# Optimization experiments

Hardware: AMD Instinct MI355X
Metric: run time of the kernel (lower is better)

## Reference

```python
import jax, jax.numpy as jnp
import numpy as np

N = 100000   # nodes
E = 3200000  # edges (avg degree 32)
IN, H, OUT = 128, 256, 40
EPS = 1e-5


def _glorot(key, fan_in, fan_out):
    s = jnp.sqrt(2.0 / (fan_in + fan_out))
    return jax.random.normal(key, (fan_in, fan_out), jnp.float32) * s


def setup_inputs() -> dict:
    key = jax.random.key(0)
    ks = jax.random.split(key, 6)
    edge_index = jax.random.randint(ks[0], (2, E), 0, N, dtype=jnp.int64)
    z = jax.random.normal(ks[1], (N, IN), jnp.float32) * 0.1
    return {
        "edge_index": edge_index,
        "z": z,
        "W1": _glorot(ks[2], IN, H), "b1": jnp.zeros((H,), jnp.float32),
        "g1": jnp.ones((H,), jnp.float32), "beta1": jnp.zeros((H,), jnp.float32),
        "W2": _glorot(ks[3], H, H), "b2": jnp.zeros((H,), jnp.float32),
        "g2": jnp.ones((H,), jnp.float32), "beta2": jnp.zeros((H,), jnp.float32),
        "W3": _glorot(ks[4], H, OUT), "b3": jnp.zeros((OUT,), jnp.float32),
    }


def _gcn_norm(edge_index):
    # add self-loops, compute symmetric normalization D^-1/2 (A+I) D^-1/2
    loops = jnp.arange(N, dtype=edge_index.dtype)
    src = jnp.concatenate([edge_index[0], loops])
    dst = jnp.concatenate([edge_index[1], loops])
    deg = jax.ops.segment_sum(jnp.ones_like(dst, jnp.float32), dst, num_segments=N)
    dinv = jnp.where(deg > 0, jax.lax.rsqrt(deg), 0.0)
    norm = dinv[src] * dinv[dst]  # [E+N]
    return src, dst, norm


def _conv(x, W, b, src, dst, norm):
    h = x @ W                              # [N, F_out]
    msg = h[src] * norm[:, None]           # gather + scale, [E+N, F_out]
    return jax.ops.segment_sum(msg, dst, num_segments=N) + b


def _bn(x, g, beta):
    m = x.mean(axis=0)
    v = x.var(axis=0)  # biased variance (training-mode BatchNorm)
    return (x - m) * jax.lax.rsqrt(v + EPS) * g + beta


def reference(edge_index, z, W1, b1, g1, beta1, W2, b2, g2, beta2, W3, b3):
    src, dst, norm = _gcn_norm(edge_index)
    x = jax.nn.relu(_bn(_conv(z, W1, b1, src, dst, norm), g1, beta1))
    x = jax.nn.relu(_bn(_conv(x, W2, b2, src, dst, norm), g2, beta2))
    return _conv(x, W3, b3, src, dst, norm)  # [N, OUT]
```

## Files before the change

### kernel.cpp

```cpp
#include <hip/hip_runtime.h>


#define NN   100000
#define NE   3200000
#define FIN  128
#define FH   256
#define FOUT 40
#define EPSV 1e-5f

#define BSH   7
#define NBKT  ((NN + 127) >> BSH)
#define CAPB  8192
#define CHNK  4096

typedef __attribute__((ext_vector_type(8))) short bf8;
typedef __attribute__((ext_vector_type(4))) float f32x4;

__device__ __forceinline__ unsigned short f2bf(float x) {
    unsigned int u = __float_as_uint(x);
    unsigned int r = u + 0x7fffu + ((u >> 16) & 1u);
    return (unsigned short)(r >> 16);
}
__device__ __forceinline__ float bf2f(unsigned short h) {
    return __uint_as_float(((unsigned int)h) << 16);
}
__device__ __forceinline__ void f2bf2(float x, unsigned short& hi, unsigned short& lo) {
    unsigned short h = f2bf(x);
    hi = h;
    lo = f2bf(x - bf2f(h));
}
__device__ __forceinline__ float ub(unsigned int u, int k) {
    return (float)((u >> (8 * k)) & 0xffu);
}
__device__ __forceinline__ float sbyte(unsigned int u, int k) {
    return (float)(int)(signed char)((u >> (8 * k)) & 0xffu);
}

__global__ __launch_bounds__(256) void k_bin(const int* __restrict__ ei,
                                             int* __restrict__ gcur,
                                             unsigned int* __restrict__ staging) {
    __shared__ int hcnt[NBKT];
    __shared__ int hbase[NBKT];
    __shared__ int sflag;
    const int tid = threadIdx.x;
    const int e0 = blockIdx.x * CHNK;
    for (int b = tid; b < NBKT; b += 256) hcnt[b] = 0;
    if (tid == 0) {
        int zz = 0;
        for (int i = 0; i < 64; i++) zz |= ei[2 * i + 1];
        sflag = (zz == 0) ? 1 : 0;
    }
    __syncthreads();
    const int f = sflag;
    for (int r = 0; r < CHNK / 256; r++) {
        int e = e0 + r * 256 + tid;
        if (e < NE) {
            int d = f ? ei[2 * (NE + e)] : ei[NE + e];
            atomicAdd(&hcnt[d >> BSH], 1);
        }
    }
    __syncthreads();
    for (int b = tid; b < NBKT; b += 256) {
        int c = hcnt[b];
        hbase[b] = c ? atomicAdd(&gcur[b], c) : 0;
    }
    __syncthreads();
    for (int b = tid; b < NBKT; b += 256) hcnt[b] = 0;
    __syncthreads();
    for (int r = 0; r < CHNK / 256; r++) {
        int e = e0 + r * 256 + tid;
        if (e < NE) {
            int s = f ? ei[2 * e] : ei[e];
            int d = f ? ei[2 * (NE + e)] : ei[NE + e];
            int b = d >> BSH;
            int loc = atomicAdd(&hcnt[b], 1);
            int pos = hbase[b] + loc;
            if (pos < CAPB)
                staging[(size_t)b * CAPB + pos] =
                    (unsigned int)s | ((unsigned int)(d & 127) << 17);
        }
    }
}

__global__ void k_bucketscan(const int* __restrict__ gcur, int* __restrict__ bbase) {
    __shared__ int sb2[2][256];
    int t = threadIdx.x;
    int base = t * 4;
    int v0 = (base + 0 < NBKT) ? gcur[base + 0] : 0;
    int v1 = (base + 1 < NBKT) ? gcur[base + 1] : 0;
    int v2 = (base + 2 < NBKT) ? gcur[base + 2] : 0;
    int v3 = (base + 3 < NBKT) ? gcur[base + 3] : 0;
    int s0 = v0, s1 = s0 + v1, s2 = s1 + v2, s3 = s2 + v3;
    sb2[0][t] = s3;
    __syncthreads();
    int pi = 0;
    for (int off = 1; off < 256; off <<= 1) {
        int x = sb2[pi][t];
        if (t >= off) x += sb2[pi][t - off];
        sb2[pi ^ 1][t] = x;
        __syncthreads();
        pi ^= 1;
    }
    int excl = sb2[pi][t] - s3;
    if (base + 0 < NBKT) bbase[base + 0] = excl;
    if (base + 1 < NBKT) bbase[base + 1] = excl + s0;
    if (base + 2 < NBKT) bbase[base + 2] = excl + s1;
    if (base + 3 < NBKT) bbase[base + 3] = excl + s2;
}

__global__ __launch_bounds__(256) void k_build(const unsigned int* __restrict__ staging,
                                               const int* __restrict__ gcur,
                                               const int* __restrict__ bbase,
                                               int* __restrict__ cntg,
                                               float* __restrict__ dinv,
                                               int* __restrict__ rowptr,
                                               int* __restrict__ csr) {
    __shared__ int lcnt[128];
    __shared__ int lscan[2][128];
    __shared__ int lcur[128];
    const int tid = threadIdx.x;
    const int b = blockIdx.x;
    const int tot = min(gcur[b], CAPB);
    const int bb = bbase[b];
    const unsigned int* st = staging + (size_t)b * CAPB;
    if (tid < 128) lcnt[tid] = 0;
    __syncthreads();
    for (int i = tid; i < tot; i += 256) {
        unsigned int v = st[i];
        atomicAdd(&lcnt[v >> 17], 1);
    }
    __syncthreads();
    int pi = 0;
    if (tid < 128) lscan[0][tid] = lcnt[tid];
    __syncthreads();
    for (int off = 1; off < 128; off <<= 1) {
        if (tid < 128) {
            int x = lscan[pi][tid];
            if (tid >= off) x += lscan[pi][tid - off];
            lscan[pi ^ 1][tid] = x;
        }
        __syncthreads();
        pi ^= 1;
    }
    if (tid < 128) {
        int c = lcnt[tid];
        int excl = lscan[pi][tid] - c;
        lcur[tid] = excl;
        int node = (b << BSH) + tid;
        if (node < NN) {
            cntg[node] = c;
            dinv[node] = rsqrtf((float)(c + 1));
            rowptr[node] = bb + excl;
        }
    }
    __syncthreads();
    for (int i = tid; i < tot; i += 256) {
        unsigned int v = st[i];
        int pos = atomicAdd(&lcur[v >> 17], 1);
        csr[bb + pos] = (int)(v & 0x1ffffu);
    }
}

__global__ void k_wprep(const float* __restrict__ W1, unsigned short* __restrict__ W1h,
                        unsigned short* __restrict__ W1l,
                        const float* __restrict__ W2, unsigned short* __restrict__ W2h,
                        unsigned short* __restrict__ W2l,
                        const float* __restrict__ W3, unsigned short* __restrict__ W3h,
                        unsigned short* __restrict__ W3l) {
    int idx = blockIdx.x * blockDim.x + threadIdx.x;
    const float* W;
    unsigned short *Wh, *Wl;
    int K, M, MP;
    if (idx < 256 * 128) {
        W = W1; Wh = W1h; Wl = W1l; K = 128; M = 256; MP = 256;
    } else if (idx < 256 * 128 + 256 * 256) {
        idx -= 256 * 128;
        W = W2; Wh = W2h; Wl = W2l; K = 256; M = 256; MP = 256;
    } else if (idx < 256 * 128 + 256 * 256 + 64 * 256) {
        idx -= 256 * 128 + 256 * 256;
        W = W3; Wh = W3h; Wl = W3l; K = 256; M = 40; MP = 64;
    } else {
        return;
    }
    int m = idx / K, k = idx - m * K;
    float v = (m < M) ? W[(size_t)k * M + m] : 0.f;
    unsigned short h, l;
    f2bf2(v, h, l);
    size_t dst = ((size_t)(k >> 5) * MP + m) * 32 + (k & 31);
    Wh[dst] = h;
    Wl[dst] = l;
}

__global__ __launch_bounds__(256) void k_zpb8(const float* __restrict__ z,
                                              const float* __restrict__ dinv,
                                              unsigned char* __restrict__ zp8,
                                              float* __restrict__ scaleZ) {
    int wv = (blockIdx.x * blockDim.x + threadIdx.x) >> 6;
    int lane = threadIdx.x & 63;
    if (wv >= NN) return;
    float2 v = *(const float2*)(z + (size_t)wv * FIN + lane * 2);
    float d = dinv[wv];
    float a0 = v.x * d, a1 = v.y * d;
    float m = fmaxf(fabsf(a0), fabsf(a1));
#pragma unroll
    for (int off = 1; off < 64; off <<= 1) m = fmaxf(m, __shfl_xor(m, off));
    float inv = m > 0.f ? 127.f / m : 0.f;
    int q0 = (int)rintf(a0 * inv), q1 = (int)rintf(a1 * inv);
    unsigned short pk = (unsigned short)((q0 & 0xff) | ((q1 & 0xff) << 8));
    *(unsigned short*)(zp8 + (size_t)wv * FIN + lane * 2) = pk;
    if (lane == 0) scaleZ[wv] = m * (1.f / 127.f);
}

__global__ __launch_bounds__(256) void k_bnr8(const unsigned short* __restrict__ x,
                                              const float* __restrict__ scale,
                                              const float* __restrict__ shift,
                                              const float* __restrict__ dinv,
                                              unsigned char* __restrict__ y8,
                                              float* __restrict__ scaleY) {
    int wv = (blockIdx.x * blockDim.x + threadIdx.x) >> 6;
    int lane = threadIdx.x & 63;
    if (wv >= NN) return;
    uint2 u = *(const uint2*)(x + (size_t)wv * 256 + lane * 4);
    float4 sc = *(const float4*)(scale + lane * 4);
    float4 sh = *(const float4*)(shift + lane * 4);
    float d = dinv[wv];
    float v0 = fmaxf(__uint_as_float(u.x << 16) * sc.x + sh.x, 0.f) * d;
    float v1 = fmaxf(__uint_as_float(u.x & 0xffff0000u) * sc.y + sh.y, 0.f) * d;
    float v2 = fmaxf(__uint_as_float(u.y << 16) * sc.z + sh.z, 0.f) * d;
    float v3 = fmaxf(__uint_as_float(u.y & 0xffff0000u) * sc.w + sh.w, 0.f) * d;
    float m = fmaxf(fmaxf(v0, v1), fmaxf(v2, v3));
#pragma unroll
    for (int off = 1; off < 64; off <<= 1) m = fmaxf(m, __shfl_xor(m, off));
    float inv = m > 0.f ? 255.f / m : 0.f;
    unsigned int q0 = (unsigned int)(v0 * inv + 0.5f);
    unsigned int q1 = (unsigned int)(v1 * inv + 0.5f);
    unsigned int q2 = (unsigned int)(v2 * inv + 0.5f);
    unsigned int q3 = (unsigned int)(v3 * inv + 0.5f);
    *(unsigned int*)(y8 + (size_t)wv * 256 + lane * 4) = q0 | (q1 << 8) | (q2 << 16) | (q3 << 24);
    if (lane == 0) scaleY[wv] = m * (1.f / 255.f);
}

template <int F, bool SIGNED>
__global__ __launch_bounds__(256) void k_agg8(const unsigned char* __restrict__ tab,
                                              const float* __restrict__ rscale,
                                              const float* __restrict__ dinv,
                                              const int* __restrict__ rowptr,
                                              const int* __restrict__ cnt,
                                              const int* __restrict__ csr,
                                              unsigned short* __restrict__ oa) {
    const int wid = threadIdx.x >> 6;
    const int lane = threadIdx.x & 63;
    const int wstep = (blockDim.x >> 6) * gridDim.x;
    constexpr int B = F / 64;
    const int off = lane * B;
    for (int row0 = blockIdx.x * (blockDim.x >> 6) + wid; row0 < NN; row0 += wstep) {
        const int row = __builtin_amdgcn_readfirstlane(row0);
        const int rp = __builtin_amdgcn_readfirstlane(rowptr[row]);
        const int cn = __builtin_amdgcn_readfirstlane(cnt[row]);
        float acc[B];
        {
            float s = rscale[row];
            if constexpr (B == 4) {
                unsigned int u = *(const unsigned int*)(tab + (size_t)row * F + off);
                acc[0] = s * ub(u, 0); acc[1] = s * ub(u, 1);
                acc[2] = s * ub(u, 2); acc[3] = s * ub(u, 3);
            } else {
                unsigned int u = *(const unsigned short*)(tab + (size_t)row * F + off);
                acc[0] = s * sbyte(u, 0); acc[1] = s * sbyte(u, 1);
            }
        }
        int e = 0;
        for (; e + 8 <= cn; e += 8) {
            int idx[8];
            float s[8];
            unsigned int u[8];
#pragma unroll
            for (int j = 0; j < 8; j++) idx[j] = csr[rp + e + j];
#pragma unroll
            for (int j = 0; j < 8; j++) s[j] = rscale[idx[j]];
#pragma unroll
            for (int j = 0; j < 8; j++) {
                if constexpr (B == 4)
                    u[j] = *(const unsigned int*)(tab + (size_t)idx[j] * F + off);
                else
                    u[j] = *(const unsigned short*)(tab + (size_t)idx[j] * F + off);
            }
#pragma unroll
            for (int j = 0; j < 8; j++) {
                if constexpr (B == 4) {
                    acc[0] += s[j] * ub(u[j], 0); acc[1] += s[j] * ub(u[j], 1);
                    acc[2] += s[j] * ub(u[j], 2); acc[3] += s[j] * ub(u[j], 3);
                } else {
                    acc[0] += s[j] * sbyte(u[j], 0); acc[1] += s[j] * sbyte(u[j], 1);
                }
            }
        }
        for (; e < cn; e++) {
            int idx = csr[rp + e];
            float s = rscale[idx];
            if constexpr (B == 4) {
                unsigned int u = *(const unsigned int*)(tab + (size_t)idx * F + off);
                acc[0] += s * ub(u, 0); acc[1] += s * ub(u, 1);
                acc[2] += s * ub(u, 2); acc[3] += s * ub(u, 3);
            } else {
                unsigned int u = *(const unsigned short*)(tab + (size_t)idx * F + off);
                acc[0] += s * sbyte(u, 0); acc[1] += s * sbyte(u, 1);
            }
        }
        float d = dinv[row];
        size_t p = (size_t)row * F + off;
        if constexpr (B == 4) {
            uint2 o;
            o.x = (unsigned int)f2bf(acc[0] * d) | ((unsigned int)f2bf(acc[1] * d) << 16);
            o.y = (unsigned int)f2bf(acc[2] * d) | ((unsigned int)f2bf(acc[3] * d) << 16);
            *(uint2*)(oa + p) = o;
        } else {
            *(unsigned int*)(oa + p) =
                (unsigned int)f2bf(acc[0] * d) | ((unsigned int)f2bf(acc[1] * d) << 16);
        }
    }
}

template <int K>
__global__ __launch_bounds__(256) void k_gemm(const unsigned short* __restrict__ A,
                                              const unsigned short* __restrict__ Wth,
                                              const unsigned short* __restrict__ Wtl,
                                              const float* __restrict__ bias,
                                              unsigned short* __restrict__ outX,
                                              float* __restrict__ s1,
                                              float* __restrict__ s2) {
    __shared__ unsigned short sA[64][40];
    const int t = threadIdx.x;
    const int w = t >> 6, lane = t & 63;
    const int quad = lane >> 4, l16 = lane & 15;
    const int rowBase = blockIdx.y * 64;
    const int colW = blockIdx.x * 128 + w * 32;
    f32x4 acc[4][2];
#pragma unroll
    for (int i = 0; i < 4; i++)
#pragma unroll
        for (int j = 0; j < 2; j++) acc[i][j] = (f32x4)0.f;

    for (int k0 = 0; k0 < K; k0 += 32) {
        int gr = rowBase + (t >> 2);
        int4 v = {0, 0, 0, 0};
        if (gr < NN) v = *(const int4*)(A + (size_t)gr * K + k0 + (t & 3) * 8);
        __syncthreads();
        *(int4*)&sA[t >> 2][(t & 3) * 8] = v;
        __syncthreads();
        const int kb = k0 >> 5;
        bf8 bh[2], bl[2];
#pragma unroll
        for (int j = 0; j < 2; j++) {
            size_t bo = ((size_t)(kb * 256 + colW + j * 16 + l16)) * 32 + quad * 8;
            bh[j] = *(const bf8*)(Wth + bo);
            bl[j] = *(const bf8*)(Wtl + bo);
        }
#pragma unroll
        for (int i = 0; i < 4; i++) {
            bf8 a = *(const bf8*)&sA[i * 16 + l16][quad * 8];
#pragma unroll
            for (int j = 0; j < 2; j++) {
                acc[i][j] = __builtin_amdgcn_mfma_f32_16x16x32_bf16(a, bh[j], acc[i][j], 0, 0, 0);
                acc[i][j] = __builtin_amdgcn_mfma_f32_16x16x32_bf16(a, bl[j], acc[i][j], 0, 0, 0);
            }
        }
    }
#pragma unroll
    for (int j = 0; j < 2; j++) {
        int col = colW + j * 16 + l16;
        float b = bias[col];
        float s1p = 0.f, s2p = 0.f;
#pragma unroll
        for (int i = 0; i < 4; i++) {
#pragma unroll
            for (int r = 0; r < 4; r++) {
                int row = rowBase + i * 16 + quad * 4 + r;
                if (row < NN) {
                    float v = acc[i][j][r] + b;
                    s1p += v;
                    s2p += v * v;
                    outX[(size_t)row * 256 + col] = f2bf(v);
                }
            }
        }
        s1p += __shfl_xor(s1p, 16); s1p += __shfl_xor(s1p, 32);
        s2p += __shfl_xor(s2p, 16); s2p += __shfl_xor(s2p, 32);
        if (quad == 0) {
            atomicAdd(&s1[col], s1p);
            atomicAdd(&s2[col], s2p);
        }
    }
}

__global__ __launch_bounds__(256) void k_mgemm3(const unsigned short* __restrict__ y2,
                                                const unsigned short* __restrict__ Wth,
                                                const unsigned short* __restrict__ Wtl,
                                                unsigned char* __restrict__ H8,
                                                float* __restrict__ scaleH) {
    __shared__ unsigned short sA[128][40];
    __shared__ float sM[128][4];
    const int t = threadIdx.x;
    const int w = t >> 6, lane = t & 63;
    const int quad = lane >> 4, l16 = lane & 15;
    const int rowBase = blockIdx.x << 7;
    f32x4 acc[8];
#pragma unroll
    for (int i = 0; i < 8; i++) acc[i] = (f32x4)0.f;

    for (int k0 = 0; k0 < 256; k0 += 32) {
        const int kb = k0 >> 5;
        int id0 = t, id1 = t + 256;
        int gr0 = rowBase + (id0 >> 2), gr1 = rowBase + (id1 >> 2);
        int4 zz = {0, 0, 0, 0};
        int4 v0 = (gr0 < NN) ? *(const int4*)(y2 + (size_t)gr0 * 256 + k0 + (id0 & 3) * 8) : zz;
        int4 v1 = (gr1 < NN) ? *(const int4*)(y2 + (size_t)gr1 * 256 + k0 + (id1 & 3) * 8) : zz;
        __syncthreads();
        *(int4*)&sA[id0 >> 2][(id0 & 3) * 8] = v0;
        *(int4*)&sA[id1 >> 2][(id1 & 3) * 8] = v1;
        __syncthreads();
        size_t bo = ((size_t)(kb * 64 + w * 16 + l16)) * 32 + quad * 8;
        bf8 bh = *(const bf8*)(Wth + bo);
        bf8 bl = *(const bf8*)(Wtl + bo);
#pragma unroll
        for (int i = 0; i < 8; i++) {
            bf8 a = *(const bf8*)&sA[i * 16 + l16][quad * 8];
            acc[i] = __builtin_amdgcn_mfma_f32_16x16x32_bf16(a, bh, acc[i], 0, 0, 0);
            acc[i] = __builtin_amdgcn_mfma_f32_16x16x32_bf16(a, bl, acc[i], 0, 0, 0);
        }
    }
#pragma unroll
    for (int i = 0; i < 8; i++) {
#pragma unroll
        for (int r = 0; r < 4; r++) {
            float m = fabsf(acc[i][r]);
            m = fmaxf(m, __shfl_xor(m, 1));
            m = fmaxf(m, __shfl_xor(m, 2));
            m = fmaxf(m, __shfl_xor(m, 4));
            m = fmaxf(m, __shfl_xor(m, 8));
            if (l16 == 0) sM[i * 16 + quad * 4 + r][w] = m;
        }
    }
    __syncthreads();
    const int col = w * 16 + l16;
#pragma unroll
    for (int i = 0; i < 8; i++) {
#pragma unroll
        for (int r = 0; r < 4; r++) {
            int rloc = i * 16 + quad * 4 + r;
            int row = rowBase + rloc;
            float m = fmaxf(fmaxf(sM[rloc][0], sM[rloc][1]), fmaxf(sM[rloc][2], sM[rloc][3]));
            float inv = m > 0.f ? 127.f / m : 0.f;
            if (row < NN) {
                int q = (int)rintf(acc[i][r] * inv);
                H8[(size_t)row * 64 + col] = (unsigned char)(q & 0xff);
                if (w == 0 && l16 == 0) scaleH[row] = m * (1.f / 127.f);
            }
        }
    }
}

__global__ __launch_bounds__(256) void k_aggfb8(const unsigned char* __restrict__ tab,
                                                const float* __restrict__ rscale,
                                                const float* __restrict__ dinv,
                                                const int* __restrict__ rowptr,
                                                const int* __restrict__ cnt,
                                                const int* __restrict__ csr,
                                                const float* __restrict__ bias,
                                                float* __restrict__ out) {
    const int wid = threadIdx.x >> 6;
    const int lane = threadIdx.x & 63;
    const int wstep = (blockDim.x >> 6) * gridDim.x;
    for (int row0 = blockIdx.x * (blockDim.x >> 6) + wid; row0 < NN; row0 += wstep) {
        const int row = __builtin_amdgcn_readfirstlane(row0);
        const int rp = __builtin_amdgcn_readfirstlane(rowptr[row]);
        const int cn = __builtin_amdgcn_readfirstlane(cnt[row]);
        float acc = rscale[row] * (float)(int)(signed char)tab[(size_t)row * 64 + lane];
        int e = 0;
        for (; e + 8 <= cn; e += 8) {
            int idx[8];
            float s[8];
            float v[8];
#pragma unroll
            for (int j = 0; j < 8; j++) idx[j] = csr[rp + e + j];
#pragma unroll
            for (int j = 0; j < 8; j++) s[j] = rscale[idx[j]];
#pragma unroll
            for (int j = 0; j < 8; j++)
                v[j] = (float)(int)(signed char)tab[(size_t)idx[j] * 64 + lane];
#pragma unroll
            for (int j = 0; j < 8; j++) acc += s[j] * v[j];
        }
        for (; e < cn; e++) {
            int idx = csr[rp + e];
            float s = rscale[idx];
            acc += s * (float)(int)(signed char)tab[(size_t)idx * 64 + lane];
        }
        if (lane < FOUT) out[(size_t)row * FOUT + lane] = acc * dinv[row] + bias[lane];
    }
}

__global__ void k_bnfold(const float* __restrict__ s1, const float* __restrict__ s2,
                         const float* __restrict__ g, const float* __restrict__ be,
                         float* __restrict__ scale, float* __restrict__ shift) {
    int c = threadIdx.x;
    if (c < 256) {
        float mean = s1[c] * (1.f / NN);
        float var = s2[c] * (1.f / NN) - mean * mean;
        float sc = g[c] * rsqrtf(var + EPSV);
        scale[c] = sc;
        shift[c] = be[c] - mean * sc;
    }
}

__global__ void k_bnr(const unsigned short* __restrict__ x,
                      const float* __restrict__ scale, const float* __restrict__ shift,
                      const float* __restrict__ dinv, unsigned short* __restrict__ oy) {
    int i = blockIdx.x * blockDim.x + threadIdx.x;
    if (i >= NN * 128) return;
    int row = i >> 7;
    int c = (i & 127) * 2;
    unsigned int u = ((const unsigned int*)x)[i];
    float x0 = __uint_as_float(u << 16);
    float x1 = __uint_as_float(u & 0xffff0000u);
    float d = dinv[row];
    float v0 = fmaxf(x0 * scale[c + 0] + shift[c + 0], 0.f) * d;
    float v1 = fmaxf(x1 * scale[c + 1] + shift[c + 1], 0.f) * d;
    ((unsigned int*)oy)[i] = (unsigned int)f2bf(v0) | ((unsigned int)f2bf(v1) << 16);
}

extern "C" void kernel_launch(void* const* d_in, const int* in_sizes, int n_in,
                              void* d_out, int out_size, void* d_ws, size_t ws_size,
                              hipStream_t stream) {
    const int* ei = (const int*)d_in[0];
    const float* z = (const float*)d_in[1];
    const float* W1 = (const float*)d_in[2];
    const float* b1 = (const float*)d_in[3];
    const float* g1 = (const float*)d_in[4];
    const float* be1 = (const float*)d_in[5];
    const float* W2 = (const float*)d_in[6];
    const float* b2 = (const float*)d_in[7];
    const float* g2 = (const float*)d_in[8];
    const float* be2 = (const float*)d_in[9];
    const float* W3 = (const float*)d_in[10];
    const float* b3 = (const float*)d_in[11];
    float* out = (float*)d_out;

    char* w = (char*)d_ws;
    size_t o = 0;
    auto take = [&](size_t bytes) {
        char* p = w + o;
        o = (o + bytes + 255) & ~(size_t)255;
        return p;
    };
    int* cnt = (int*)take((size_t)NN * 4);
    int* rowptr = (int*)take((size_t)NN * 4);
    int* gcur = (int*)take(NBKT * 4);
    int* bbase = (int*)take(NBKT * 4);
    int* csr = (int*)take((size_t)NE * 4);
    unsigned int* staging = (unsigned int*)take((size_t)NBKT * CAPB * 4);
    float* dinv = (float*)take((size_t)NN * 4);
    float* stat = (float*)take(4 * 256 * 4);
    float* sc1 = (float*)take(256 * 4);
    float* sh1 = (float*)take(256 * 4);
    float* sc2 = (float*)take(256 * 4);
    float* sh2 = (float*)take(256 * 4);
    unsigned short* Wt1h = (unsigned short*)take(256 * 128 * 2);
    unsigned short* Wt1l = (unsigned short*)take(256 * 128 * 2);
    unsigned short* Wt2h = (unsigned short*)take(256 * 256 * 2);
    unsigned short* Wt2l = (unsigned short*)take(256 * 256 * 2);
    unsigned short* Wt3h = (unsigned short*)take(64 * 256 * 2);
    unsigned short* Wt3l = (unsigned short*)take(64 * 256 * 2);
    unsigned char* zp8 = (unsigned char*)take((size_t)NN * FIN);
    unsigned char* y1_8 = (unsigned char*)take((size_t)NN * FH);
    unsigned char* H8 = (unsigned char*)take((size_t)NN * 64);
    float* scaleZ = (float*)take((size_t)NN * 4);
    float* scaleY = (float*)take((size_t)NN * 4);
    float* scaleH = (float*)take((size_t)NN * 4);
    unsigned short* P1 = (unsigned short*)take((size_t)NN * 256 * 2);
    unsigned short* P2 = (unsigned short*)take((size_t)NN * 512 * 2);

    unsigned short* a1 = P1;
    unsigned short* x1 = P2;
    unsigned short* a2 = P2 + (size_t)NN * 256;
    unsigned short* x2 = P1;
    unsigned short* y2 = P2;
    float* s1a = stat, *s2a = stat + 256, *s1b = stat + 512, *s2b = stat + 768;

    hipMemsetAsync(gcur, 0, NBKT * 4, stream);
    hipMemsetAsync(stat, 0, 4 * 256 * 4, stream);

    k_bin<<<(NE + CHNK - 1) / CHNK, 256, 0, stream>>>(ei, gcur, staging);
    k_bucketscan<<<1, 256, 0, stream>>>(gcur, bbase);
    k_build<<<NBKT, 256, 0, stream>>>(staging, gcur, bbase, cnt, dinv, rowptr, csr);

    k_wprep<<<(256 * 128 + 256 * 256 + 64 * 256 + 255) / 256, 256, 0, stream>>>(
        W1, Wt1h, Wt1l, W2, Wt2h, Wt2l, W3, Wt3h, Wt3l);

    const int GR = (NN + 63) / 64;
    const int WV = (NN + 3) / 4;

    k_zpb8<<<WV, 256, 0, stream>>>(z, dinv, zp8, scaleZ);
    k_agg8<128, true><<<2560, 256, 0, stream>>>(zp8, scaleZ, dinv, rowptr, cnt, csr, a1);
    k_gemm<128><<<dim3(2, GR), 256, 0, stream>>>(a1, Wt1h, Wt1l, b1, x1, s1a, s2a);
    k_bnfold<<<1, 256, 0, stream>>>(s1a, s2a, g1, be1, sc1, sh1);
    k_bnr8<<<WV, 256, 0, stream>>>(x1, sc1, sh1, dinv, y1_8, scaleY);

    k_agg8<256, false><<<2560, 256, 0, stream>>>(y1_8, scaleY, dinv, rowptr, cnt, csr, a2);
    k_gemm<256><<<dim3(2, GR), 256, 0, stream>>>(a2, Wt2h, Wt2l, b2, x2, s1b, s2b);
    k_bnfold<<<1, 256, 0, stream>>>(s1b, s2b, g2, be2, sc2, sh2);
    k_bnr<<<(NN * 128 + 255) / 256, 256, 0, stream>>>(x2, sc2, sh2, dinv, y2);

    k_mgemm3<<<NBKT, 256, 0, stream>>>(y2, Wt3h, Wt3l, H8, scaleH);
    k_aggfb8<<<2560, 256, 0, stream>>>(H8, scaleH, dinv, rowptr, cnt, csr, b3, out);
}
```

Before: 815.8 us.

## Fuse BN folding into consumers and pipeline two-row edge aggregation

Removes the k_bnfold launches by computing BN scale/shift inline in k_bnr8 and k_mgemm3. The second BN+ReLU pass (k_bnr) is fused into the final GEMM's A-tile load, which drops a full intermediate write and read. The aggregation kernels now process two rows per wave with double-buffered 8-edge batches so gathers overlap with FMAs. The padded batches waste some loads on self-rows, and register pressure goes up.

```diff
diff --git a/kernel.cpp b/kernel.cpp
--- a/kernel.cpp
+++ b/kernel.cpp
@@ -212,22 +212,34 @@
 }
 
 __global__ __launch_bounds__(256) void k_bnr8(const unsigned short* __restrict__ x,
-                                              const float* __restrict__ scale,
-                                              const float* __restrict__ shift,
+                                              const float* __restrict__ s1,
+                                              const float* __restrict__ s2,
+                                              const float* __restrict__ g,
+                                              const float* __restrict__ be,
                                               const float* __restrict__ dinv,
                                               unsigned char* __restrict__ y8,
                                               float* __restrict__ scaleY) {
     int wv = (blockIdx.x * blockDim.x + threadIdx.x) >> 6;
     int lane = threadIdx.x & 63;
     if (wv >= NN) return;
+    float4 m1 = *(const float4*)(s1 + lane * 4);
+    float4 m2 = *(const float4*)(s2 + lane * 4);
+    float4 gg = *(const float4*)(g + lane * 4);
+    float4 bb = *(const float4*)(be + lane * 4);
+    float mx = m1.x * (1.f / NN), my = m1.y * (1.f / NN);
+    float mz = m1.z * (1.f / NN), mw = m1.w * (1.f / NN);
+    float scx = gg.x * rsqrtf(m2.x * (1.f / NN) - mx * mx + EPSV);
+    float scy = gg.y * rsqrtf(m2.y * (1.f / NN) - my * my + EPSV);
+    float scz = gg.z * rsqrtf(m2.z * (1.f / NN) - mz * mz + EPSV);
+    float scw = gg.w * rsqrtf(m2.w * (1.f / NN) - mw * mw + EPSV);
+    float shx = bb.x - mx * scx, shy = bb.y - my * scy;
+    float shz = bb.z - mz * scz, shw = bb.w - mw * scw;
     uint2 u = *(const uint2*)(x + (size_t)wv * 256 + lane * 4);
-    float4 sc = *(const float4*)(scale + lane * 4);
-    float4 sh = *(const float4*)(shift + lane * 4);
     float d = dinv[wv];
-    float v0 = fmaxf(__uint_as_float(u.x << 16) * sc.x + sh.x, 0.f) * d;
-    float v1 = fmaxf(__uint_as_float(u.x & 0xffff0000u) * sc.y + sh.y, 0.f) * d;
-    float v2 = fmaxf(__uint_as_float(u.y << 16) * sc.z + sh.z, 0.f) * d;
-    float v3 = fmaxf(__uint_as_float(u.y & 0xffff0000u) * sc.w + sh.w, 0.f) * d;
+    float v0 = fmaxf(__uint_as_float(u.x << 16) * scx + shx, 0.f) * d;
+    float v1 = fmaxf(__uint_as_float(u.x & 0xffff0000u) * scy + shy, 0.f) * d;
+    float v2 = fmaxf(__uint_as_float(u.y << 16) * scz + shz, 0.f) * d;
+    float v3 = fmaxf(__uint_as_float(u.y & 0xffff0000u) * scw + shw, 0.f) * d;
     float m = fmaxf(fmaxf(v0, v1), fmaxf(v2, v3));
 #pragma unroll
     for (int off = 1; off < 64; off <<= 1) m = fmaxf(m, __shfl_xor(m, off));
@@ -241,7 +253,7 @@
 }
 
 template <int F, bool SIGNED>
-__global__ __launch_bounds__(256) void k_agg8(const unsigned char* __restrict__ tab,
+__global__ __launch_bounds__(256) void k_agg2(const unsigned char* __restrict__ tab,
                                               const float* __restrict__ rscale,
                                               const float* __restrict__ dinv,
                                               const int* __restrict__ rowptr,
@@ -253,60 +265,49 @@
     const int wstep = (blockDim.x >> 6) * gridDim.x;
     constexpr int B = F / 64;
     const int off = lane * B;
-    for (int row0 = blockIdx.x * (blockDim.x >> 6) + wid; row0 < NN; row0 += wstep) {
-        const int row = __builtin_amdgcn_readfirstlane(row0);
-        const int rp = __builtin_amdgcn_readfirstlane(rowptr[row]);
-        const int cn = __builtin_amdgcn_readfirstlane(cnt[row]);
-        float acc[B];
-        {
-            float s = rscale[row];
+    const int NP = (NN + 1) / 2;
+
+    auto LOADB = [&](int row, int rp, int cn, int b, float* sc, unsigned int* u) {
+#pragma unroll
+        for (int j = 0; j < 8; j++) {
+            int e = b * 8 + j;
+            int ci = (e < cn) ? csr[rp + e] : row;
+            sc[j] = (e < cn) ? rscale[ci] : 0.f;
+            if constexpr (B == 4)
+                u[j] = *(const unsigned int*)(tab + (size_t)ci * F + off);
+            else
+                u[j] = *(const unsigned short*)(tab + (size_t)ci * F + off);
+        }
+    };
+    auto FMAB = [&](float* acc, const float* sc, const unsigned int* u) {
+#pragma unroll
+        for (int j = 0; j < 8; j++) {
             if constexpr (B == 4) {
-                unsigned int u = *(const unsigned int*)(tab + (size_t)row * F + off);
-                acc[0] = s * ub(u, 0); acc[1] = s * ub(u, 1);
-                acc[2] = s * ub(u, 2); acc[3] = s * ub(u, 3);
+                acc[0] += sc[j] * (SIGNED ? sbyte(u[j], 0) : ub(u[j], 0));
+                acc[1] += sc[j] * (SIGNED ? sbyte(u[j], 1) : ub(u[j], 1));
+                acc[2] += sc[j] * (SIGNED ? sbyte(u[j], 2) : ub(u[j], 2));
+                acc[3] += sc[j] * (SIGNED ? sbyte(u[j], 3) : ub(u[j], 3));
             } else {
-                unsigned int u = *(const unsigned short*)(tab + (size_t)row * F + off);
-                acc[0] = s * sbyte(u, 0); acc[1] = s * sbyte(u, 1);
+                acc[0] += sc[j] * (SIGNED ? sbyte(u[j], 0) : ub(u[j], 0));
+                acc[1] += sc[j] * (SIGNED ? sbyte(u[j], 1) : ub(u[j], 1));
             }
         }
-        int e = 0;
-        for (; e + 8 <= cn; e += 8) {
-            int idx[8];
-            float s[8];
-            unsigned int u[8];
-#pragma unroll
-            for (int j = 0; j < 8; j++) idx[j] = csr[rp + e + j];
-#pragma unroll
-            for (int j = 0; j < 8; j++) s[j] = rscale[idx[j]];
-#pragma unroll
-            for (int j = 0; j < 8; j++) {
-                if constexpr (B == 4)
-                    u[j] = *(const unsigned int*)(tab + (size_t)idx[j] * F + off);
-                else
-                    u[j] = *(const unsigned short*)(tab + (size_t)idx[j] * F + off);
-            }
-#pragma unroll
-            for (int j = 0; j < 8; j++) {
-                if constexpr (B == 4) {
-                    acc[0] += s[j] * ub(u[j], 0); acc[1] += s[j] * ub(u[j], 1);
-                    acc[2] += s[j] * ub(u[j], 2); acc[3] += s[j] * ub(u[j], 3);
-                } else {
-                    acc[0] += s[j] * sbyte(u[j], 0); acc[1] += s[j] * sbyte(u[j], 1);
-                }
-            }
-        }
-        for (; e < cn; e++) {
-            int idx = csr[rp + e];
-            float s = rscale[idx];
-            if constexpr (B == 4) {
-                unsigned int u = *(const unsigned int*)(tab + (size_t)idx * F + off);
-                acc[0] += s * ub(u, 0); acc[1] += s * ub(u, 1);
-                acc[2] += s * ub(u, 2); acc[3] += s * ub(u, 3);
-            } else {
-                unsigned int u = *(const unsigned short*)(tab + (size_t)idx * F + off);
-                acc[0] += s * sbyte(u, 0); acc[1] += s * sbyte(u, 1);
-            }
-        }
+    };
+    auto SELF = [&](int row, float* acc) {
+        float s = rscale[row];
+        if constexpr (B == 4) {
+            unsigned int u = *(const unsigned int*)(tab + (size_t)row * F + off);
+            acc[0] = s * (SIGNED ? sbyte(u, 0) : ub(u, 0));
+            acc[1] = s * (SIGNED ? sbyte(u, 1) : ub(u, 1));
+            acc[2] = s * (SIGNED ? sbyte(u, 2) : ub(u, 2));
+            acc[3] = s * (SIGNED ? sbyte(u, 3) : ub(u, 3));
+        } else {
+            unsigned int u = *(const unsigned short*)(tab + (size_t)row * F + off);
+            acc[0] = s * (SIGNED ? sbyte(u, 0) : ub(u, 0));
+            acc[1] = s * (SIGNED ? sbyte(u, 1) : ub(u, 1));
+        }
+    };
+    auto STORE = [&](int row, const float* acc) {
         float d = dinv[row];
         size_t p = (size_t)row * F + off;
         if constexpr (B == 4) {
@@ -318,6 +319,44 @@
             *(unsigned int*)(oa + p) =
                 (unsigned int)f2bf(acc[0] * d) | ((unsigned int)f2bf(acc[1] * d) << 16);
         }
+    };
+
+    for (int p0 = blockIdx.x * (blockDim.x >> 6) + wid; p0 < NP; p0 += wstep) {
+        const int rA = __builtin_amdgcn_readfirstlane(p0 * 2);
+        const int rB = min(rA + 1, NN - 1);
+        const int rpA = __builtin_amdgcn_readfirstlane(rowptr[rA]);
+        const int cnA = __builtin_amdgcn_readfirstlane(cnt[rA]);
+        const int rpB = __builtin_amdgcn_readfirstlane(rowptr[rB]);
+        const int cnB = __builtin_amdgcn_readfirstlane(cnt[rB]);
+        float accA[B], accB[B];
+        SELF(rA, accA);
+        SELF(rB, accB);
+        const int nb = max((cnA + 7) >> 3, (cnB + 7) >> 3);
+        if (nb > 0) {
+            float scA0[8], scB0[8], scA1[8], scB1[8];
+            unsigned int uA0[8], uB0[8], uA1[8], uB1[8];
+            LOADB(rA, rpA, cnA, 0, scA0, uA0);
+            LOADB(rB, rpB, cnB, 0, scB0, uB0);
+            int b = 0;
+            while (true) {
+                bool more = (b + 1 < nb);
+                if (more) LOADB(rA, rpA, cnA, b + 1, scA1, uA1);
+                FMAB(accA, scA0, uA0);
+                if (more) LOADB(rB, rpB, cnB, b + 1, scB1, uB1);
+                FMAB(accB, scB0, uB0);
+                if (!more) break;
+                b++;
+                bool more2 = (b + 1 < nb);
+                if (more2) LOADB(rA, rpA, cnA, b + 1, scA0, uA0);
+                FMAB(accA, scA1, uA1);
+                if (more2) LOADB(rB, rpB, cnB, b + 1, scB0, uB0);
+                FMAB(accB, scB1, uB1);
+                if (!more2) break;
+                b++;
+            }
+        }
+        STORE(rA, accA);
+        if (rB != rA) STORE(rB, accB);
     }
 }
 
@@ -393,31 +432,68 @@
     }
 }
 
-__global__ __launch_bounds__(256) void k_mgemm3(const unsigned short* __restrict__ y2,
+__device__ __forceinline__ unsigned int bn2(unsigned int w, float sc0, float sh0,
+                                            float sc1, float sh1, float d) {
+    float x0 = __uint_as_float(w << 16);
+    float x1 = __uint_as_float(w & 0xffff0000u);
+    float y0 = fmaxf(x0 * sc0 + sh0, 0.f) * d;
+    float y1 = fmaxf(x1 * sc1 + sh1, 0.f) * d;
+    return (unsigned int)f2bf(y0) | ((unsigned int)f2bf(y1) << 16);
+}
+
+__global__ __launch_bounds__(256) void k_mgemm3(const unsigned short* __restrict__ x2,
+                                                const float* __restrict__ s1,
+                                                const float* __restrict__ s2,
+                                                const float* __restrict__ g,
+                                                const float* __restrict__ be,
                                                 const unsigned short* __restrict__ Wth,
                                                 const unsigned short* __restrict__ Wtl,
+                                                const float* __restrict__ dinv,
                                                 unsigned char* __restrict__ H8,
                                                 float* __restrict__ scaleH) {
     __shared__ unsigned short sA[128][40];
     __shared__ float sM[128][4];
+    __shared__ float sSC[256];
+    __shared__ float sSH[256];
     const int t = threadIdx.x;
     const int w = t >> 6, lane = t & 63;
     const int quad = lane >> 4, l16 = lane & 15;
     const int rowBase = blockIdx.x << 7;
+    {
+        float mean = s1[t] * (1.f / NN);
+        float var = s2[t] * (1.f / NN) - mean * mean;
+        float sc = g[t] * rsqrtf(var + EPSV);
+        sSC[t] = sc;
+        sSH[t] = be[t] - mean * sc;
+    }
     f32x4 acc[8];
 #pragma unroll
     for (int i = 0; i < 8; i++) acc[i] = (f32x4)0.f;
+
+    const int gr0 = rowBase + (t >> 2);
+    const int gr1 = gr0 + 64;
+    const float dA = (gr0 < NN) ? dinv[gr0] : 0.f;
+    const float dB = (gr1 < NN) ? dinv[gr1] : 0.f;
+    const int cb = (t & 3) * 8;
+    __syncthreads();
 
     for (int k0 = 0; k0 < 256; k0 += 32) {
         const int kb = k0 >> 5;
-        int id0 = t, id1 = t + 256;
-        int gr0 = rowBase + (id0 >> 2), gr1 = rowBase + (id1 >> 2);
         int4 zz = {0, 0, 0, 0};
-        int4 v0 = (gr0 < NN) ? *(const int4*)(y2 + (size_t)gr0 * 256 + k0 + (id0 & 3) * 8) : zz;
-        int4 v1 = (gr1 < NN) ? *(const int4*)(y2 + (size_t)gr1 * 256 + k0 + (id1 & 3) * 8) : zz;
+        int4 v0 = (gr0 < NN) ? *(const int4*)(x2 + (size_t)gr0 * 256 + k0 + cb) : zz;
+        int4 v1 = (gr1 < NN) ? *(const int4*)(x2 + (size_t)gr1 * 256 + k0 + cb) : zz;
+        const int c = k0 + cb;
+        v0.x = bn2(v0.x, sSC[c + 0], sSH[c + 0], sSC[c + 1], sSH[c + 1], dA);
+        v0.y = bn2(v0.y, sSC[c + 2], sSH[c + 2], sSC[c + 3], sSH[c + 3], dA);
+        v0.z = bn2(v0.z, sSC[c + 4], sSH[c + 4], sSC[c + 5], sSH[c + 5], dA);
+        v0.w = bn2(v0.w, sSC[c + 6], sSH[c + 6], sSC[c + 7], sSH[c + 7], dA);
+        v1.x = bn2(v1.x, sSC[c + 0], sSH[c + 0], sSC[c + 1], sSH[c + 1], dB);
+        v1.y = bn2(v1.y, sSC[c + 2], sSH[c + 2], sSC[c + 3], sSH[c + 3], dB);
+        v1.z = bn2(v1.z, sSC[c + 4], sSH[c + 4], sSC[c + 5], sSH[c + 5], dB);
+        v1.w = bn2(v1.w, sSC[c + 6], sSH[c + 6], sSC[c + 7], sSH[c + 7], dB);
         __syncthreads();
-        *(int4*)&sA[id0 >> 2][(id0 & 3) * 8] = v0;
-        *(int4*)&sA[id1 >> 2][(id1 & 3) * 8] = v1;
+        *(int4*)&sA[t >> 2][cb] = v0;
+        *(int4*)&sA[(t >> 2) + 64][cb] = v1;
         __syncthreads();
         size_t bo = ((size_t)(kb * 64 + w * 16 + l16)) * 32 + quad * 8;
         bf8 bh = *(const bf8*)(Wth + bo);
@@ -460,7 +536,7 @@
     }
 }
 
-__global__ __launch_bounds__(256) void k_aggfb8(const unsigned char* __restrict__ tab,
+__global__ __launch_bounds__(256) void k_aggfb2(const unsigned char* __restrict__ tab,
                                                 const float* __restrict__ rscale,
                                                 const float* __restrict__ dinv,
                                                 const int* __restrict__ rowptr,
@@ -471,62 +547,61 @@
     const int wid = threadIdx.x >> 6;
     const int lane = threadIdx.x & 63;
     const int wstep = (blockDim.x >> 6) * gridDim.x;
-    for (int row0 = blockIdx.x * (blockDim.x >> 6) + wid; row0 < NN; row0 += wstep) {
-        const int row = __builtin_amdgcn_readfirstlane(row0);
-        const int rp = __builtin_amdgcn_readfirstlane(rowptr[row]);
-        const int cn = __builtin_amdgcn_readfirstlane(cnt[row]);
-        float acc = rscale[row] * (float)(int)(signed char)tab[(size_t)row * 64 + lane];
-        int e = 0;
-        for (; e + 8 <= cn; e += 8) {
-            int idx[8];
-            float s[8];
-            float v[8];
-#pragma unroll
-            for (int j = 0; j < 8; j++) idx[j] = csr[rp + e + j];
-#pragma unroll
-            for (int j = 0; j < 8; j++) s[j] = rscale[idx[j]];
-#pragma unroll
-            for (int j = 0; j < 8; j++)
-                v[j] = (float)(int)(signed char)tab[(size_t)idx[j] * 64 + lane];
-#pragma unroll
-            for (int j = 0; j < 8; j++) acc += s[j] * v[j];
-        }
-        for (; e < cn; e++) {
-            int idx = csr[rp + e];
-            float s = rscale[idx];
-            acc += s * (float)(int)(signed char)tab[(size_t)idx * 64 + lane];
-        }
-        if (lane < FOUT) out[(size_t)row * FOUT + lane] = acc * dinv[row] + bias[lane];
-    }
-}
-
-__global__ void k_bnfold(const float* __restrict__ s1, const float* __restrict__ s2,
-                         const float* __restrict__ g, const float* __restrict__ be,
-                         float* __restrict__ scale, float* __restrict__ shift) {
-    int c = threadIdx.x;
-    if (c < 256) {
-        float mean = s1[c] * (1.f / NN);
-        float var = s2[c] * (1.f / NN) - mean * mean;
-        float sc = g[c] * rsqrtf(var + EPSV);
-        scale[c] = sc;
-        shift[c] = be[c] - mean * sc;
-    }
-}
-
-__global__ void k_bnr(const unsigned short* __restrict__ x,
-                      const float* __restrict__ scale, const float* __restrict__ shift,
-                      const float* __restrict__ dinv, unsigned short* __restrict__ oy) {
-    int i = blockIdx.x * blockDim.x + threadIdx.x;
-    if (i >= NN * 128) return;
-    int row = i >> 7;
-    int c = (i & 127) * 2;
-    unsigned int u = ((const unsigned int*)x)[i];
-    float x0 = __uint_as_float(u << 16);
-    float x1 = __uint_as_float(u & 0xffff0000u);
-    float d = dinv[row];
-    float v0 = fmaxf(x0 * scale[c + 0] + shift[c + 0], 0.f) * d;
-    float v1 = fmaxf(x1 * scale[c + 1] + shift[c + 1], 0.f) * d;
-    ((unsigned int*)oy)[i] = (unsigned int)f2bf(v0) | ((unsigned int)f2bf(v1) << 16);
+    const int NP = (NN + 1) / 2;
+    const float bv = (lane < FOUT) ? bias[lane] : 0.f;
+
+    auto LOADB = [&](int row, int rp, int cn, int b, float* sc, int* u) {
+#pragma unroll
+        for (int j = 0; j < 8; j++) {
+            int e = b * 8 + j;
+            int ci = (e < cn) ? csr[rp + e] : row;
+            sc[j] = (e < cn) ? rscale[ci] : 0.f;
+            u[j] = (int)(signed char)tab[(size_t)ci * 64 + lane];
+        }
+    };
+    auto FMAB = [&](float& acc, const float* sc, const int* u) {
+#pragma unroll
+        for (int j = 0; j < 8; j++) acc += sc[j] * (float)u[j];
+    };
+
+    for (int p0 = blockIdx.x * (blockDim.x >> 6) + wid; p0 < NP; p0 += wstep) {
+        const int rA = __builtin_amdgcn_readfirstlane(p0 * 2);
+        const int rB = min(rA + 1, NN - 1);
+        const int rpA = __builtin_amdgcn_readfirstlane(rowptr[rA]);
+        const int cnA = __builtin_amdgcn_readfirstlane(cnt[rA]);
+        const int rpB = __builtin_amdgcn_readfirstlane(rowptr[rB]);
+        const int cnB = __builtin_amdgcn_readfirstlane(cnt[rB]);
+        float accA = rscale[rA] * (float)(int)(signed char)tab[(size_t)rA * 64 + lane];
+        float accB = rscale[rB] * (float)(int)(signed char)tab[(size_t)rB * 64 + lane];
+        const int nb = max((cnA + 7) >> 3, (cnB + 7) >> 3);
+        if (nb > 0) {
+            float scA0[8], scB0[8], scA1[8], scB1[8];
+            int uA0[8], uB0[8], uA1[8], uB1[8];
+            LOADB(rA, rpA, cnA, 0, scA0, uA0);
+            LOADB(rB, rpB, cnB, 0, scB0, uB0);
+            int b = 0;
+            while (true) {
+                bool more = (b + 1 < nb);
+                if (more) LOADB(rA, rpA, cnA, b + 1, scA1, uA1);
+                FMAB(accA, scA0, uA0);
+                if (more) LOADB(rB, rpB, cnB, b + 1, scB1, uB1);
+                FMAB(accB, scB0, uB0);
+                if (!more) break;
+                b++;
+                bool more2 = (b + 1 < nb);
+                if (more2) LOADB(rA, rpA, cnA, b + 1, scA0, uA0);
+                FMAB(accA, scA1, uA1);
+                if (more2) LOADB(rB, rpB, cnB, b + 1, scB0, uB0);
+                FMAB(accB, scB1, uB1);
+                if (!more2) break;
+                b++;
+            }
+        }
+        if (lane < FOUT) {
+            out[(size_t)rA * FOUT + lane] = accA * dinv[rA] + bv;
+            if (rB != rA) out[(size_t)rB * FOUT + lane] = accB * dinv[rB] + bv;
+        }
+    }
 }
 
 extern "C" void kernel_launch(void* const* d_in, const int* in_sizes, int n_in,
@@ -557,14 +632,10 @@
     int* rowptr = (int*)take((size_t)NN * 4);
     int* gcur = (int*)take(NBKT * 4);
     int* bbase = (int*)take(NBKT * 4);
-    int* csr = (int*)take((size_t)NE * 4);
+    int* csr = (int*)take((size_t)NE * 4 + 256);
     unsigned int* staging = (unsigned int*)take((size_t)NBKT * CAPB * 4);
     float* dinv = (float*)take((size_t)NN * 4);
     float* stat = (float*)take(4 * 256 * 4);
-    float* sc1 = (float*)take(256 * 4);
-    float* sh1 = (float*)take(256 * 4);
-    float* sc2 = (float*)take(256 * 4);
-    float* sh2 = (float*)take(256 * 4);
     unsigned short* Wt1h = (unsigned short*)take(256 * 128 * 2);
     unsigned short* Wt1l = (unsigned short*)take(256 * 128 * 2);
     unsigned short* Wt2h = (unsigned short*)take(256 * 256 * 2);
@@ -584,7 +655,6 @@
     unsigned short* x1 = P2;
     unsigned short* a2 = P2 + (size_t)NN * 256;
     unsigned short* x2 = P1;
-    unsigned short* y2 = P2;
     float* s1a = stat, *s2a = stat + 256, *s1b = stat + 512, *s2b = stat + 768;
 
     hipMemsetAsync(gcur, 0, NBKT * 4, stream);
@@ -601,16 +671,13 @@
     const int WV = (NN + 3) / 4;
 
     k_zpb8<<<WV, 256, 0, stream>>>(z, dinv, zp8, scaleZ);
-    k_agg8<128, true><<<2560, 256, 0, stream>>>(zp8, scaleZ, dinv, rowptr, cnt, csr, a1);
+    k_agg2<128, true><<<2560, 256, 0, stream>>>(zp8, scaleZ, dinv, rowptr, cnt, csr, a1);
     k_gemm<128><<<dim3(2, GR), 256, 0, stream>>>(a1, Wt1h, Wt1l, b1, x1, s1a, s2a);
-    k_bnfold<<<1, 256, 0, stream>>>(s1a, s2a, g1, be1, sc1, sh1);
-    k_bnr8<<<WV, 256, 0, stream>>>(x1, sc1, sh1, dinv, y1_8, scaleY);
-
-    k_agg8<256, false><<<2560, 256, 0, stream>>>(y1_8, scaleY, dinv, rowptr, cnt, csr, a2);
+    k_bnr8<<<WV, 256, 0, stream>>>(x1, s1a, s2a, g1, be1, dinv, y1_8, scaleY);
+
+    k_agg2<256, false><<<2560, 256, 0, stream>>>(y1_8, scaleY, dinv, rowptr, cnt, csr, a2);
     k_gemm<256><<<dim3(2, GR), 256, 0, stream>>>(a2, Wt2h, Wt2l, b2, x2, s1b, s2b);
-    k_bnfold<<<1, 256, 0, stream>>>(s1b, s2b, g2, be2, sc2, sh2);
-    k_bnr<<<(NN * 128 + 255) / 256, 256, 0, stream>>>(x2, sc2, sh2, dinv, y2);
-
-    k_mgemm3<<<NBKT, 256, 0, stream>>>(y2, Wt3h, Wt3l, H8, scaleH);
-    k_aggfb8<<<2560, 256, 0, stream>>>(H8, scaleH, dinv, rowptr, cnt, csr, b3, out);
-}
+
+    k_mgemm3<<<NBKT, 256, 0, stream>>>(x2, s1b, s2b, g2, be2, Wt3h, Wt3l, dinv, H8, scaleH);
+    k_aggfb2<<<2560, 256, 0, stream>>>(H8, scaleH, dinv, rowptr, cnt, csr, b3, out);
+}
```

New measurement: 996.0 us. 1.22x slower.

## Fuse BN fold into consumers and BN+ReLU+scaling into final GEMM load

Applied to the files above, without the earlier changes.

Removes the two k_bnfold launches by computing BatchNorm scale/shift inline in k_bnr8 and in k_mgemm3. Removes the standalone k_bnr pass for layer 2 by applying BN, ReLU and dinv scaling while staging x2 tiles into shared memory in k_mgemm3, which avoids writing and re-reading a bf16 NxH intermediate. Also lowers the aggregation grid size from 2560 to 2048 and pads the csr allocation. The cost is redundant per-wave/per-block recomputation of the BN fold and extra ALU work in the GEMM load path.

```diff
diff --git a/kernel.cpp b/kernel.cpp
--- a/kernel.cpp
+++ b/kernel.cpp
@@ -212,22 +212,34 @@
 }
 
 __global__ __launch_bounds__(256) void k_bnr8(const unsigned short* __restrict__ x,
-                                              const float* __restrict__ scale,
-                                              const float* __restrict__ shift,
+                                              const float* __restrict__ s1,
+                                              const float* __restrict__ s2,
+                                              const float* __restrict__ g,
+                                              const float* __restrict__ be,
                                               const float* __restrict__ dinv,
                                               unsigned char* __restrict__ y8,
                                               float* __restrict__ scaleY) {
     int wv = (blockIdx.x * blockDim.x + threadIdx.x) >> 6;
     int lane = threadIdx.x & 63;
     if (wv >= NN) return;
+    float4 m1 = *(const float4*)(s1 + lane * 4);
+    float4 m2 = *(const float4*)(s2 + lane * 4);
+    float4 gg = *(const float4*)(g + lane * 4);
+    float4 bb = *(const float4*)(be + lane * 4);
+    float mx = m1.x * (1.f / NN), my = m1.y * (1.f / NN);
+    float mz = m1.z * (1.f / NN), mw = m1.w * (1.f / NN);
+    float scx = gg.x * rsqrtf(m2.x * (1.f / NN) - mx * mx + EPSV);
+    float scy = gg.y * rsqrtf(m2.y * (1.f / NN) - my * my + EPSV);
+    float scz = gg.z * rsqrtf(m2.z * (1.f / NN) - mz * mz + EPSV);
+    float scw = gg.w * rsqrtf(m2.w * (1.f / NN) - mw * mw + EPSV);
+    float shx = bb.x - mx * scx, shy = bb.y - my * scy;
+    float shz = bb.z - mz * scz, shw = bb.w - mw * scw;
     uint2 u = *(const uint2*)(x + (size_t)wv * 256 + lane * 4);
-    float4 sc = *(const float4*)(scale + lane * 4);
-    float4 sh = *(const float4*)(shift + lane * 4);
     float d = dinv[wv];
-    float v0 = fmaxf(__uint_as_float(u.x << 16) * sc.x + sh.x, 0.f) * d;
-    float v1 = fmaxf(__uint_as_float(u.x & 0xffff0000u) * sc.y + sh.y, 0.f) * d;
-    float v2 = fmaxf(__uint_as_float(u.y << 16) * sc.z + sh.z, 0.f) * d;
-    float v3 = fmaxf(__uint_as_float(u.y & 0xffff0000u) * sc.w + sh.w, 0.f) * d;
+    float v0 = fmaxf(__uint_as_float(u.x << 16) * scx + shx, 0.f) * d;
+    float v1 = fmaxf(__uint_as_float(u.x & 0xffff0000u) * scy + shy, 0.f) * d;
+    float v2 = fmaxf(__uint_as_float(u.y << 16) * scz + shz, 0.f) * d;
+    float v3 = fmaxf(__uint_as_float(u.y & 0xffff0000u) * scw + shw, 0.f) * d;
     float m = fmaxf(fmaxf(v0, v1), fmaxf(v2, v3));
 #pragma unroll
     for (int off = 1; off < 64; off <<= 1) m = fmaxf(m, __shfl_xor(m, off));
@@ -393,31 +405,68 @@
     }
 }
 
-__global__ __launch_bounds__(256) void k_mgemm3(const unsigned short* __restrict__ y2,
+__device__ __forceinline__ unsigned int bn2(unsigned int w, float sc0, float sh0,
+                                            float sc1, float sh1, float d) {
+    float x0 = __uint_as_float(w << 16);
+    float x1 = __uint_as_float(w & 0xffff0000u);
+    float y0 = fmaxf(x0 * sc0 + sh0, 0.f) * d;
+    float y1 = fmaxf(x1 * sc1 + sh1, 0.f) * d;
+    return (unsigned int)f2bf(y0) | ((unsigned int)f2bf(y1) << 16);
+}
+
+__global__ __launch_bounds__(256) void k_mgemm3(const unsigned short* __restrict__ x2,
+                                                const float* __restrict__ s1,
+                                                const float* __restrict__ s2,
+                                                const float* __restrict__ g,
+                                                const float* __restrict__ be,
                                                 const unsigned short* __restrict__ Wth,
                                                 const unsigned short* __restrict__ Wtl,
+                                                const float* __restrict__ dinv,
                                                 unsigned char* __restrict__ H8,
                                                 float* __restrict__ scaleH) {
     __shared__ unsigned short sA[128][40];
     __shared__ float sM[128][4];
+    __shared__ float sSC[256];
+    __shared__ float sSH[256];
     const int t = threadIdx.x;
     const int w = t >> 6, lane = t & 63;
     const int quad = lane >> 4, l16 = lane & 15;
     const int rowBase = blockIdx.x << 7;
+    {
+        float mean = s1[t] * (1.f / NN);
+        float var = s2[t] * (1.f / NN) - mean * mean;
+        float sc = g[t] * rsqrtf(var + EPSV);
+        sSC[t] = sc;
+        sSH[t] = be[t] - mean * sc;
+    }
     f32x4 acc[8];
 #pragma unroll
     for (int i = 0; i < 8; i++) acc[i] = (f32x4)0.f;
+
+    const int gr0 = rowBase + (t >> 2);
+    const int gr1 = gr0 + 64;
+    const float dA = (gr0 < NN) ? dinv[gr0] : 0.f;
+    const float dB = (gr1 < NN) ? dinv[gr1] : 0.f;
+    const int cb = (t & 3) * 8;
+    __syncthreads();
 
     for (int k0 = 0; k0 < 256; k0 += 32) {
         const int kb = k0 >> 5;
-        int id0 = t, id1 = t + 256;
-        int gr0 = rowBase + (id0 >> 2), gr1 = rowBase + (id1 >> 2);
         int4 zz = {0, 0, 0, 0};
-        int4 v0 = (gr0 < NN) ? *(const int4*)(y2 + (size_t)gr0 * 256 + k0 + (id0 & 3) * 8) : zz;
-        int4 v1 = (gr1 < NN) ? *(const int4*)(y2 + (size_t)gr1 * 256 + k0 + (id1 & 3) * 8) : zz;
+        int4 v0 = (gr0 < NN) ? *(const int4*)(x2 + (size_t)gr0 * 256 + k0 + cb) : zz;
+        int4 v1 = (gr1 < NN) ? *(const int4*)(x2 + (size_t)gr1 * 256 + k0 + cb) : zz;
+        const int c = k0 + cb;
+        v0.x = bn2(v0.x, sSC[c + 0], sSH[c + 0], sSC[c + 1], sSH[c + 1], dA);
+        v0.y = bn2(v0.y, sSC[c + 2], sSH[c + 2], sSC[c + 3], sSH[c + 3], dA);
+        v0.z = bn2(v0.z, sSC[c + 4], sSH[c + 4], sSC[c + 5], sSH[c + 5], dA);
+        v0.w = bn2(v0.w, sSC[c + 6], sSH[c + 6], sSC[c + 7], sSH[c + 7], dA);
+        v1.x = bn2(v1.x, sSC[c + 0], sSH[c + 0], sSC[c + 1], sSH[c + 1], dB);
+        v1.y = bn2(v1.y, sSC[c + 2], sSH[c + 2], sSC[c + 3], sSH[c + 3], dB);
+        v1.z = bn2(v1.z, sSC[c + 4], sSH[c + 4], sSC[c + 5], sSH[c + 5], dB);
+        v1.w = bn2(v1.w, sSC[c + 6], sSH[c + 6], sSC[c + 7], sSH[c + 7], dB);
         __syncthreads();
-        *(int4*)&sA[id0 >> 2][(id0 & 3) * 8] = v0;
-        *(int4*)&sA[id1 >> 2][(id1 & 3) * 8] = v1;
+        *(int4*)&sA[t >> 2][cb] = v0;
+        *(int4*)&sA[(t >> 2) + 64][cb] = v1;
         __syncthreads();
         size_t bo = ((size_t)(kb * 64 + w * 16 + l16)) * 32 + quad * 8;
         bf8 bh = *(const bf8*)(Wth + bo);
@@ -500,35 +549,6 @@
     }
 }
 
-__global__ void k_bnfold(const float* __restrict__ s1, const float* __restrict__ s2,
-                         const float* __restrict__ g, const float* __restrict__ be,
-                         float* __restrict__ scale, float* __restrict__ shift) {
-    int c = threadIdx.x;
-    if (c < 256) {
-        float mean = s1[c] * (1.f / NN);
-        float var = s2[c] * (1.f / NN) - mean * mean;
-        float sc = g[c] * rsqrtf(var + EPSV);
-        scale[c] = sc;
-        shift[c] = be[c] - mean * sc;
-    }
-}
-
-__global__ void k_bnr(const unsigned short* __restrict__ x,
-                      const float* __restrict__ scale, const float* __restrict__ shift,
-                      const float* __restrict__ dinv, unsigned short* __restrict__ oy) {
-    int i = blockIdx.x * blockDim.x + threadIdx.x;
-    if (i >= NN * 128) return;
-    int row = i >> 7;
-    int c = (i & 127) * 2;
-    unsigned int u = ((const unsigned int*)x)[i];
-    float x0 = __uint_as_float(u << 16);
-    float x1 = __uint_as_float(u & 0xffff0000u);
-    float d = dinv[row];
-    float v0 = fmaxf(x0 * scale[c + 0] + shift[c + 0], 0.f) * d;
-    float v1 = fmaxf(x1 * scale[c + 1] + shift[c + 1], 0.f) * d;
-    ((unsigned int*)oy)[i] = (unsigned int)f2bf(v0) | ((unsigned int)f2bf(v1) << 16);
-}
-
 extern "C" void kernel_launch(void* const* d_in, const int* in_sizes, int n_in,
                               void* d_out, int out_size, void* d_ws, size_t ws_size,
                               hipStream_t stream) {
@@ -557,14 +577,10 @@
     int* rowptr = (int*)take((size_t)NN * 4);
     int* gcur = (int*)take(NBKT * 4);
     int* bbase = (int*)take(NBKT * 4);
-    int* csr = (int*)take((size_t)NE * 4);
+    int* csr = (int*)take((size_t)NE * 4 + 256);
     unsigned int* staging = (unsigned int*)take((size_t)NBKT * CAPB * 4);
     float* dinv = (float*)take((size_t)NN * 4);
     float* stat = (float*)take(4 * 256 * 4);
-    float* sc1 = (float*)take(256 * 4);
-    float* sh1 = (float*)take(256 * 4);
-    float* sc2 = (float*)take(256 * 4);
-    float* sh2 = (float*)take(256 * 4);
     unsigned short* Wt1h = (unsigned short*)take(256 * 128 * 2);
     unsigned short* Wt1l = (unsigned short*)take(256 * 128 * 2);
     unsigned short* Wt2h = (unsigned short*)take(256 * 256 * 2);
@@ -584,7 +600,6 @@
     unsigned short* x1 = P2;
     unsigned short* a2 = P2 + (size_t)NN * 256;
     unsigned short* x2 = P1;
-    unsigned short* y2 = P2;
     float* s1a = stat, *s2a = stat + 256, *s1b = stat + 512, *s2b = stat + 768;
 
     hipMemsetAsync(gcur, 0, NBKT * 4, stream);
@@ -601,16 +616,13 @@
     const int WV = (NN + 3) / 4;
 
     k_zpb8<<<WV, 256, 0, stream>>>(z, dinv, zp8, scaleZ);
-    k_agg8<128, true><<<2560, 256, 0, stream>>>(zp8, scaleZ, dinv, rowptr, cnt, csr, a1);
+    k_agg8<128, true><<<2048, 256, 0, stream>>>(zp8, scaleZ, dinv, rowptr, cnt, csr, a1);
     k_gemm<128><<<dim3(2, GR), 256, 0, stream>>>(a1, Wt1h, Wt1l, b1, x1, s1a, s2a);
-    k_bnfold<<<1, 256, 0, stream>>>(s1a, s2a, g1, be1, sc1, sh1);
-    k_bnr8<<<WV, 256, 0, stream>>>(x1, sc1, sh1, dinv, y1_8, scaleY);
-
-    k_agg8<256, false><<<2560, 256, 0, stream>>>(y1_8, scaleY, dinv, rowptr, cnt, csr, a2);
+    k_bnr8<<<WV, 256, 0, stream>>>(x1, s1a, s2a, g1, be1, dinv, y1_8, scaleY);
+
+    k_agg8<256, false><<<2048, 256, 0, stream>>>(y1_8, scaleY, dinv, rowptr, cnt, csr, a2);
     k_gemm<256><<<dim3(2, GR), 256, 0, stream>>>(a2, Wt2h, Wt2l, b2, x2, s1b, s2b);
-    k_bnfold<<<1, 256, 0, stream>>>(s1b, s2b, g2, be2, sc2, sh2);
-    k_bnr<<<(NN * 128 + 255) / 256, 256, 0, stream>>>(x2, sc2, sh2, dinv, y2);
-
-    k_mgemm3<<<NBKT, 256, 0, stream>>>(y2, Wt3h, Wt3l, H8, scaleH);
-    k_aggfb8<<<2560, 256, 0, stream>>>(H8, scaleH, dinv, rowptr, cnt, csr, b3, out);
-}
+
+    k_mgemm3<<<NBKT, 256, 0, stream>>>(x2, s1b, s2b, g2, be2, Wt3h, Wt3l, dinv, H8, scaleH);
+    k_aggfb8<<<2048, 256, 0, stream>>>(H8, scaleH, dinv, rowptr, cnt, csr, b3, out);
+}
```

Result: faster. 793.2 us (-2.8%).
